# Kernel tuning notes

Measured on AMD Instinct MI355X. Metric: run time of the kernel, lower is better.

## Reference

```python
import jax, jax.numpy as jnp
import numpy as np

N = 100000      # nodes
E = 1600000     # edges (avg degree 16)
EMB = 128
L = 3           # num_layers
NUM_OPS = 64
MAX_BW = 64     # max_bitwidth
P = 4           # max_num_params


def setup_inputs() -> dict:
    key = jax.random.key(0)
    ks = jax.random.split(key, 24)
    w = lambda k, s: jax.random.normal(k, s, jnp.float32) * 0.05
    return {
        "ops": jax.random.randint(ks[0], (N,), 0, NUM_OPS),
        "params": jax.random.randint(ks[1], (N, P), 0, MAX_BW),
        "edge_src": jax.random.randint(ks[2], (E,), 0, N),
        "edge_dst": jax.random.randint(ks[3], (E,), 0, N),
        "op_emb_table": w(ks[4], (NUM_OPS, EMB)),
        "param_emb_table": w(ks[5], (MAX_BW, EMB)),
        "opmlp_w1": w(ks[6], ((1 + P) * EMB, EMB)), "opmlp_b1": w(ks[7], (EMB,)),
        "opmlp_w2": w(ks[8], (EMB, EMB)), "opmlp_b2": w(ks[9], (EMB,)),
        "conv_w": w(ks[10], (L, EMB, EMB)), "conv_b": w(ks[11], (L, EMB)),
        "mlp_w1": w(ks[12], (L * EMB, EMB)), "mlp_b1": w(ks[13], (EMB,)),
        "mlp_w2": w(ks[14], (EMB, EMB)), "mlp_b2": w(ks[15], (EMB,)),
        "mlpinv_w1": w(ks[16], (L * EMB, EMB)), "mlpinv_b1": w(ks[17], (EMB,)),
        "mlpinv_w2": w(ks[18], (EMB, EMB)), "mlpinv_b2": w(ks[19], (EMB,)),
        "comb_w": w(ks[20], (2 * EMB, EMB)), "comb_b": w(ks[21], (EMB,)),
    }


def _lrelu(x):
    return jax.nn.leaky_relu(x)  # slope 0.01, matches nn.LeakyReLU default


def _gin_mean(feat, src, dst, w, b):
    # DGL GINConv(aggregator='mean', eps=0): apply_func(feat + mean_in_neighbors(feat))
    n = feat.shape[0]
    msg = jax.ops.segment_sum(feat[src], dst, num_segments=n)           # [N, EMB]
    deg = jax.ops.segment_sum(jnp.ones(src.shape, feat.dtype), dst, num_segments=n)
    agg = msg / jnp.maximum(deg, 1.0)[:, None]
    return _lrelu((feat + agg) @ w + b)


def reference(ops, params, edge_src, edge_dst,
              op_emb_table, param_emb_table,
              opmlp_w1, opmlp_b1, opmlp_w2, opmlp_b2,
              conv_w, conv_b,
              mlp_w1, mlp_b1, mlp_w2, mlp_b2,
              mlpinv_w1, mlpinv_b1, mlpinv_w2, mlpinv_b2,
              comb_w, comb_b):
    n = ops.shape[0]
    # OpEmb: cat([op_emb] + per-param embs) -> MLP
    op_e = op_emb_table[ops]                               # [N, EMB]
    par_e = param_emb_table[params].reshape(n, -1)         # [N, P*EMB]
    h = jnp.concatenate([op_e, par_e], axis=1)
    h = _lrelu(h @ opmlp_w1 + opmlp_b1) @ opmlp_w2 + opmlp_b2
    states = h
    states_inv = h  # op_emb called twice on same inputs in the original

    conv_outs = []
    for i in range(L):
        states = _gin_mean(states, edge_src, edge_dst, conv_w[i], conv_b[i])
        conv_outs.append(states.sum(axis=0))
    final_sum = states.sum(axis=0)

    conv_outs_inv = []
    for i in range(L):
        states_inv = _gin_mean(states_inv, edge_dst, edge_src, conv_w[i], conv_b[i])
        # NOTE: original code appends states.sum(dim=0) (the final forward states),
        # not states_inv -- faithfully reproduced.
        conv_outs_inv.append(final_sum)

    g_emb = _lrelu(jnp.concatenate(conv_outs) @ mlp_w1 + mlp_b1) @ mlp_w2 + mlp_b2
    g_inv_emb = _lrelu(jnp.concatenate(conv_outs_inv) @ mlpinv_w1 + mlpinv_b1) @ mlpinv_w2 + mlpinv_b2

    out1 = jnp.concatenate([g_emb, g_inv_emb]) @ comb_w + comb_b          # [EMB]
    out2 = jnp.concatenate([states, states_inv], axis=1) @ comb_w + comb_b  # [N, EMB]
    return (out1, out2)
```

## Files before the change

kernel.cpp:

```cpp
#include <hip/hip_runtime.h>


typedef unsigned int  uint;
typedef unsigned short ushort;
typedef float  f32x4  __attribute__((ext_vector_type(4)));
typedef short  bf16x8 __attribute__((ext_vector_type(8)));

#define ABITS 9
#define CAPB  12288
#define CHUNK 2048

__device__ __forceinline__ float lrelu(float x) { return x > 0.0f ? x : 0.01f * x; }
__device__ __forceinline__ ushort f2b(float x) {
    uint u = __float_as_uint(x);
    return (ushort)((u + 0x7fffu + ((u >> 16) & 1u)) >> 16);
}
__device__ __forceinline__ float lof(uint u) { return __uint_as_float(u << 16); }
__device__ __forceinline__ float hif(uint u) { return __uint_as_float(u & 0xffff0000u); }

__global__ void tables_kernel(const float* __restrict__ opT, const float* __restrict__ parT,
                              const float* __restrict__ W1, float* __restrict__ A)
{
    int b = blockIdx.x;
    int t = b >> 6, v = b & 63, j = threadIdx.x;
    const float* emb = (t == 0 ? opT : parT) + v * 128;
    const float* w = W1 + (size_t)t * 128 * 128;
    float acc = 0.f;
    for (int k = 0; k < 128; ++k) acc += emb[k] * w[k * 128 + j];
    A[(size_t)b * 128 + j] = acc;
}

__global__ void prep_w(const float* __restrict__ convw, const float* __restrict__ ow2,
                       const float* __restrict__ cw, ushort* __restrict__ Wt)
{
    int t = blockIdx.x * 256 + threadIdx.x;
    int img = t >> 14, idx = t & 16383;
    int k = idx >> 7, c = idx & 127;
    const float* src;
    if (img < 3)      src = convw + img * 16384;
    else if (img == 3) src = ow2;
    else              src = cw + (img - 4) * 16384;
    float v = src[k * 128 + c];
    int byteoff = (img << 15) + (c << 8) + ((((k >> 3) ^ (c & 7)) << 4)) + ((k & 7) << 1);
    Wt[byteoff >> 1] = f2b(v);
}

__global__ __launch_bounds__(256) void binpass_kernel(
    const int* __restrict__ esrc, const int* __restrict__ edst, int E, int nb,
    int* __restrict__ gcur, uint2* __restrict__ binbuf)
{
    __shared__ int hist[448];
    __shared__ int lstart[448];
    __shared__ int gbase[448];
    __shared__ int lcur[448];
    __shared__ int gsum[8];
    __shared__ uint sKey[CHUNK * 2];
    __shared__ uint sPay[CHUNK * 2];
    __shared__ ushort sBin[CHUNK * 2];
    int tid = threadIdx.x, lane = tid & 63;
    int nb2 = nb * 2;

    for (int chunk = blockIdx.x; (size_t)chunk * CHUNK < (size_t)E; chunk += gridDim.x) {
        int base = chunk * CHUNK;
        int cnt = min(CHUNK, E - base);
        for (int i = tid; i < 448; i += 256) hist[i] = 0;
        __syncthreads();
        int s[8], d[8];
        #pragma unroll
        for (int i = 0; i < 8; ++i) {
            int idx = i * 256 + tid;
            if (idx < cnt) {
                s[i] = esrc[base + idx];
                d[i] = edst[base + idx];
                atomicAdd(&hist[d[i] >> ABITS], 1);
                atomicAdd(&hist[nb + (s[i] >> ABITS)], 1);
            } else s[i] = -1;
        }
        __syncthreads();
        #pragma unroll
        for (int k = 0; k < 2; ++k) {
            int idx = k * 256 + tid;
            int v = (idx < 448) ? hist[idx] : 0;
            int p = v;
            #pragma unroll
            for (int sh = 1; sh < 64; sh <<= 1) { int t = __shfl_up(p, sh, 64); if (lane >= sh) p += t; }
            if (idx < 448) {
                lstart[idx] = p - v;
                if (lane == 63) gsum[idx >> 6] = p;
            }
        }
        __syncthreads();
        if (tid == 0) { int run = 0; for (int g = 0; g < 7; ++g) { int t = gsum[g]; gsum[g] = run; run += t; } }
        __syncthreads();
        #pragma unroll
        for (int k = 0; k < 2; ++k) {
            int idx = k * 256 + tid;
            if (idx < 448) lstart[idx] += gsum[idx >> 6];
        }
        __syncthreads();
        for (int i = tid; i < nb2; i += 256) {
            int h = hist[i];
            gbase[i] = h ? atomicAdd(&gcur[i], h) : 0;
            lcur[i] = lstart[i];
        }
        __syncthreads();
        #pragma unroll
        for (int i = 0; i < 8; ++i) {
            if (s[i] >= 0) {
                int bf = d[i] >> ABITS;
                int p = atomicAdd(&lcur[bf], 1);
                sKey[p] = (uint)d[i]; sPay[p] = (uint)s[i]; sBin[p] = (ushort)bf;
                int bi = nb + (s[i] >> ABITS);
                int q = atomicAdd(&lcur[bi], 1);
                sKey[q] = (uint)s[i]; sPay[q] = (uint)d[i]; sBin[q] = (ushort)bi;
            }
        }
        __syncthreads();
        int total = 2 * cnt;
        for (int p = tid; p < total; p += 256) {
            int b = sBin[p];
            int pos = gbase[b] + (p - lstart[b]);
            if (pos < CAPB) binbuf[(size_t)b * CAPB + pos] = make_uint2(sKey[p], sPay[p]);
        }
        __syncthreads();
    }
}

__global__ __launch_bounds__(256) void csrpass_kernel(
    const uint2* __restrict__ binbuf, const int* __restrict__ gcur, int nb, int N,
    int* __restrict__ csr_f, int* __restrict__ off_f, int* __restrict__ cnt_f,
    int* __restrict__ csr_i, int* __restrict__ off_i, int* __restrict__ cnt_i)
{
    __shared__ int hist[512];
    __shared__ int loff[512];
    __shared__ int cur[512];
    __shared__ int gsum[8];
    int b = blockIdx.x;
    int dir = (b >= nb) ? 1 : 0;
    int binLocal = dir ? b - nb : b;
    int node0 = binLocal << ABITS;
    int nn = min(512, N - node0);
    int tid = threadIdx.x, lane = tid & 63;
    int total = min(gcur[b], CAPB);
    const uint2* seg = binbuf + (size_t)b * CAPB;
    int* csr = dir ? csr_i : csr_f;
    int* off = dir ? off_i : off_f;
    int* cnt = dir ? cnt_i : cnt_f;

    for (int i = tid; i < 512; i += 256) hist[i] = 0;
    __syncthreads();
    for (int e = tid; e < total; e += 256) {
        uint2 kp = seg[e];
        atomicAdd(&hist[kp.x - (uint)node0], 1);
    }
    __syncthreads();
    #pragma unroll
    for (int k = 0; k < 2; ++k) {
        int idx = k * 256 + tid;
        int v = hist[idx];
        int p = v;
        #pragma unroll
        for (int sh = 1; sh < 64; sh <<= 1) { int t = __shfl_up(p, sh, 64); if (lane >= sh) p += t; }
        loff[idx] = p - v;
        if (lane == 63) gsum[idx >> 6] = p;
    }
    __syncthreads();
    if (tid == 0) { int run = 0; for (int g = 0; g < 8; ++g) { int t = gsum[g]; gsum[g] = run; run += t; } }
    __syncthreads();
    #pragma unroll
    for (int k = 0; k < 2; ++k) {
        int idx = k * 256 + tid;
        loff[idx] += gsum[idx >> 6];
    }
    __syncthreads();
    int csrBase = binLocal * CAPB;
    for (int i = tid; i < 512; i += 256) {
        cur[i] = loff[i];
        if (i < nn) { off[node0 + i] = csrBase + loff[i]; cnt[node0 + i] = hist[i]; }
    }
    __syncthreads();
    int* csrSeg = csr + csrBase;
    for (int e = tid; e < total; e += 256) {
        uint2 kp = seg[e];
        int p = atomicAdd(&cur[kp.x - (uint)node0], 1);
        csrSeg[p] = (int)(kp.y << 8);
    }
}

__global__ __launch_bounds__(256, 8) void agg2_kernel(
    const ushort* __restrict__ Sf, const ushort* __restrict__ Si,
    const int* __restrict__ csr_f, const int* __restrict__ off_f, const int* __restrict__ cnt_f,
    const int* __restrict__ csr_i, const int* __restrict__ off_i, const int* __restrict__ cnt_i,
    ushort* __restrict__ msgf, ushort* __restrict__ msgi, int N)
{
    int gw = (blockIdx.x * 256 + threadIdx.x) >> 6;
    int lane = threadIdx.x & 63;
    int dir = 0, g = gw;
    if (g >= N) { dir = 1; g -= N; if (g >= N) return; }
    const char* Sp = (const char*)(dir ? Si : Sf);
    const int* csr = dir ? csr_i : csr_f;
    int off = (dir ? off_i : off_f)[g];
    int deg = (dir ? cnt_i : cnt_f)[g];
    int half = lane >> 5;
    int lb = (lane & 31) << 3;

    float a0 = 0.f, a1 = 0.f, a2 = 0.f, a3 = 0.f;
    int d = 0;
    for (; d + 8 <= deg; d += 8) {
        int b0 = csr[off + d + 0 + half];
        int b1 = csr[off + d + 2 + half];
        int b2 = csr[off + d + 4 + half];
        int b3 = csr[off + d + 6 + half];
        uint2 v0 = *(const uint2*)(Sp + (uint)(b0 + lb));
        uint2 v1 = *(const uint2*)(Sp + (uint)(b1 + lb));
        uint2 v2 = *(const uint2*)(Sp + (uint)(b2 + lb));
        uint2 v3 = *(const uint2*)(Sp + (uint)(b3 + lb));
        a0 += (lof(v0.x) + lof(v1.x)) + (lof(v2.x) + lof(v3.x));
        a1 += (hif(v0.x) + hif(v1.x)) + (hif(v2.x) + hif(v3.x));
        a2 += (lof(v0.y) + lof(v1.y)) + (lof(v2.y) + lof(v3.y));
        a3 += (hif(v0.y) + hif(v1.y)) + (hif(v2.y) + hif(v3.y));
    }
    for (; d + 2 <= deg; d += 2) {
        int b = csr[off + d + half];
        uint2 v = *(const uint2*)(Sp + (uint)(b + lb));
        a0 += lof(v.x); a1 += hif(v.x); a2 += lof(v.y); a3 += hif(v.y);
    }
    if (d < deg && half == 0) {
        int b = csr[off + d];
        uint2 v = *(const uint2*)(Sp + (uint)(b + lb));
        a0 += lof(v.x); a1 += hif(v.x); a2 += lof(v.y); a3 += hif(v.y);
    }
    a0 += __shfl_xor(a0, 32);
    a1 += __shfl_xor(a1, 32);
    a2 += __shfl_xor(a2, 32);
    a3 += __shfl_xor(a3, 32);
    float invd = 1.0f / fmaxf((float)deg, 1.0f);
    uint2 self = *(const uint2*)(Sp + ((size_t)g << 8) + lb);
    a0 = lof(self.x) + a0 * invd;
    a1 = hif(self.x) + a1 * invd;
    a2 = lof(self.y) + a2 * invd;
    a3 = hif(self.y) + a3 * invd;
    if (half == 0) {
        uint2 pk;
        pk.x = (uint)f2b(a0) | ((uint)f2b(a1) << 16);
        pk.y = (uint)f2b(a2) | ((uint)f2b(a3) << 16);
        *(uint2*)((char*)(dir ? msgi : msgf) + ((size_t)g << 8) + lb) = pk;
    }
}

__device__ __forceinline__ void stage_w(const ushort* __restrict__ img, ushort* ldsW, int tid)
{
    const uint4* s = (const uint4*)img;
    uint4* d = (uint4*)ldsW;
    #pragma unroll
    for (int i = 0; i < 4; ++i) d[tid + (i << 9)] = s[tid + (i << 9)];
}

__global__ __launch_bounds__(512, 8) void gemm2_kernel(
    const ushort* __restrict__ msgf, const ushort* __restrict__ msgi,
    ushort* __restrict__ Sf_out, ushort* __restrict__ Si_out,
    const ushort* __restrict__ Wimg, const float* __restrict__ bias,
    float* __restrict__ colsum, int N)
{
    __shared__ __align__(16) ushort ldsW[16384];
    __shared__ float ldsCS[128];
    int tid = threadIdx.x, lane = tid & 63, w = tid >> 6;
    bool fwd = (blockIdx.x & 1) == 0;
    int node0 = (blockIdx.x >> 1) << 7;
    const ushort* msg = fwd ? msgf : msgi;
    ushort* Sout = fwd ? Sf_out : Si_out;

    stage_w(Wimg, ldsW, tid);
    if (fwd && tid < 128) ldsCS[tid] = 0.f;
    __syncthreads();

    int l15 = lane & 15, lg = lane >> 4;
    int node = node0 + (w << 4) + l15;
    int gr = min(node, N - 1);
    const char* Bb = (const char*)msg + ((size_t)gr << 8);

    f32x4 acc[8];
    #pragma unroll
    for (int i = 0; i < 8; ++i) acc[i] = f32x4{0.f, 0.f, 0.f, 0.f};
    #pragma unroll
    for (int kk = 0; kk < 4; ++kk) {
        bf16x8 bfr = *(const bf16x8*)(Bb + (((kk << 2) + lg) << 4));
        #pragma unroll
        for (int ct = 0; ct < 8; ++ct) {
            int c = (ct << 4) + l15;
            const char* Ab = (const char*)ldsW + c * 256;
            bf16x8 af = *(const bf16x8*)(Ab + ((((kk << 2) + lg) << 4) ^ ((c & 7) << 4)));
            acc[ct] = __builtin_amdgcn_mfma_f32_16x16x32_bf16(af, bfr, acc[ct], 0, 0, 0);
        }
    }

    bool valid = node < N;
    #pragma unroll
    for (int ct = 0; ct < 8; ++ct) {
        int ch0 = (ct << 4) + (lg << 2);
        float4 bb = *(const float4*)(bias + ch0);
        float o0 = lrelu(acc[ct][0] + bb.x);
        float o1 = lrelu(acc[ct][1] + bb.y);
        float o2 = lrelu(acc[ct][2] + bb.z);
        float o3 = lrelu(acc[ct][3] + bb.w);
        if (valid) {
            uint2 pk;
            pk.x = (uint)f2b(o0) | ((uint)f2b(o1) << 16);
            pk.y = (uint)f2b(o2) | ((uint)f2b(o3) << 16);
            *(uint2*)((char*)Sout + ((size_t)node << 8) + (ch0 << 1)) = pk;
        }
        if (fwd) {
            float c0 = valid ? o0 : 0.f, c1 = valid ? o1 : 0.f;
            float c2 = valid ? o2 : 0.f, c3 = valid ? o3 : 0.f;
            #pragma unroll
            for (int m = 1; m < 16; m <<= 1) {
                c0 += __shfl_xor(c0, m);
                c1 += __shfl_xor(c1, m);
                c2 += __shfl_xor(c2, m);
                c3 += __shfl_xor(c3, m);
            }
            if (l15 == 0) {
                atomicAdd(&ldsCS[ch0 + 0], c0);
                atomicAdd(&ldsCS[ch0 + 1], c1);
                atomicAdd(&ldsCS[ch0 + 2], c2);
                atomicAdd(&ldsCS[ch0 + 3], c3);
            }
        }
    }
    if (fwd) {
        __syncthreads();
        if (tid < 128) atomicAdd(&colsum[tid], ldsCS[tid]);
    }
}

__global__ __launch_bounds__(512, 4) void opemb_fused(
    const int* __restrict__ ops, const int* __restrict__ params,
    const float* __restrict__ Atab, const float* __restrict__ b1,
    const ushort* __restrict__ W2img, const float* __restrict__ b2,
    ushort* __restrict__ S0, int N)
{
    __shared__ __align__(16) ushort ldsW[16384];
    __shared__ __align__(16) ushort ldsA[16384];
    int tid = threadIdx.x, lane = tid & 63, w = tid >> 6;
    int node0 = blockIdx.x << 7;

    stage_w(W2img, ldsW, tid);

    int r = tid >> 2, sub = tid & 3;
    int g = node0 + r;
    float4 acc4[8];
    if (g < N) {
        int op = ops[g];
        const float4* T = (const float4*)(Atab + ((size_t)op << 7) + (sub << 5));
        #pragma unroll
        for (int q = 0; q < 8; ++q) acc4[q] = T[q];
        #pragma unroll
        for (int p = 0; p < 4; ++p) {
            int pv = params[(g << 2) + p];
            const float4* Tp = (const float4*)(Atab + ((size_t)((p + 1) * 64 + pv) << 7) + (sub << 5));
            #pragma unroll
            for (int q = 0; q < 8; ++q) {
                float4 u = Tp[q];
                acc4[q].x += u.x; acc4[q].y += u.y; acc4[q].z += u.z; acc4[q].w += u.w;
            }
        }
        const float4* Bv = (const float4*)(b1 + (sub << 5));
        #pragma unroll
        for (int q = 0; q < 8; ++q) {
            float4 bb = Bv[q];
            acc4[q].x = lrelu(acc4[q].x + bb.x);
            acc4[q].y = lrelu(acc4[q].y + bb.y);
            acc4[q].z = lrelu(acc4[q].z + bb.z);
            acc4[q].w = lrelu(acc4[q].w + bb.w);
        }
    } else {
        #pragma unroll
        for (int q = 0; q < 8; ++q) acc4[q] = make_float4(0.f, 0.f, 0.f, 0.f);
    }
    int akey = r & 7;
    #pragma unroll
    for (int q2 = 0; q2 < 4; ++q2) {
        int ch = (sub << 2) + q2;
        float4 a = acc4[q2 * 2], b = acc4[q2 * 2 + 1];
        uint4 pk;
        pk.x = (uint)f2b(a.x) | ((uint)f2b(a.y) << 16);
        pk.y = (uint)f2b(a.z) | ((uint)f2b(a.w) << 16);
        pk.z = (uint)f2b(b.x) | ((uint)f2b(b.y) << 16);
        pk.w = (uint)f2b(b.z) | ((uint)f2b(b.w) << 16);
        *(uint4*)((char*)ldsA + r * 256 + ((ch ^ akey) << 4)) = pk;
    }
    __syncthreads();

    int l15 = lane & 15, lg = lane >> 4;
    int node = node0 + (w << 4) + l15;
    int brow = (w << 4) + l15;
    const char* Bb = (const char*)ldsA + brow * 256;
    int bkey = (brow & 7) << 4;
    f32x4 acc[8];
    #pragma unroll
    for (int i = 0; i < 8; ++i) acc[i] = f32x4{0.f, 0.f, 0.f, 0.f};
    #pragma unroll
    for (int kk = 0; kk < 4; ++kk) {
        bf16x8 bfr = *(const bf16x8*)(Bb + ((((kk << 2) + lg) << 4) ^ bkey));
        #pragma unroll
        for (int ct = 0; ct < 8; ++ct) {
            int c = (ct << 4) + l15;
            const char* Ab = (const char*)ldsW + c * 256;
            bf16x8 af = *(const bf16x8*)(Ab + ((((kk << 2) + lg) << 4) ^ ((c & 7) << 4)));
            acc[ct] = __builtin_amdgcn_mfma_f32_16x16x32_bf16(af, bfr, acc[ct], 0, 0, 0);
        }
    }
    if (node < N) {
        #pragma unroll
        for (int ct = 0; ct < 8; ++ct) {
            int ch0 = (ct << 4) + (lg << 2);
            float4 bb = *(const float4*)(b2 + ch0);
            uint2 pk;
            pk.x = (uint)f2b(acc[ct][0] + bb.x) | ((uint)f2b(acc[ct][1] + bb.y) << 16);
            pk.y = (uint)f2b(acc[ct][2] + bb.z) | ((uint)f2b(acc[ct][3] + bb.w) << 16);
            *(uint2*)((char*)S0 + ((size_t)node << 8) + (ch0 << 1)) = pk;
        }
    }
}

__device__ __forceinline__ void final_body(
    float* lds, const float* __restrict__ convsum,
    const float* __restrict__ mw1, const float* __restrict__ mb1,
    const float* __restrict__ mw2, const float* __restrict__ mb2,
    const float* __restrict__ iw1, const float* __restrict__ ib1,
    const float* __restrict__ iw2, const float* __restrict__ ib2,
    const float* __restrict__ cw, const float* __restrict__ cb,
    float* __restrict__ out1)
{
    float* x  = lds;
    float* pa = lds + 384;
    float* pb = lds + 896;
    float* t1 = lds + 1408;
    float* t2 = lds + 1536;
    int tid = threadIdx.x, j = tid & 127, s = tid >> 7;
    if (tid < 384) x[tid] = convsum[tid];
    __syncthreads();
    float a = 0.f, c = 0.f;
    for (int k = s * 96; k < s * 96 + 96; ++k) {
        a += x[k] * mw1[k * 128 + j];
        c += x[256 + (k & 127)] * iw1[k * 128 + j];
    }
    pa[tid] = a; pb[tid] = c;
    __syncthreads();
    if (s == 0) {
        t1[j] = lrelu(pa[j] + pa[128 + j] + pa[256 + j] + pa[384 + j] + mb1[j]);
        t2[j] = lrelu(pb[j] + pb[128 + j] + pb[256 + j] + pb[384 + j] + ib1[j]);
    }
    __syncthreads();
    float b = 0.f, d = 0.f;
    for (int k = s * 32; k < s * 32 + 32; ++k) {
        b += t1[k] * mw2[k * 128 + j];
        d += t2[k] * iw2[k * 128 + j];
    }
    pa[tid] = b; pb[tid] = d;
    __syncthreads();
    if (s == 0) {
        t1[j] = pa[j] + pa[128 + j] + pa[256 + j] + pa[384 + j] + mb2[j];
        t2[j] = pb[j] + pb[128 + j] + pb[256 + j] + pb[384 + j] + ib2[j];
    }
    __syncthreads();
    float e = 0.f;
    for (int k = s * 32; k < s * 32 + 32; ++k)
        e += t1[k] * cw[k * 128 + j] + t2[k] * cw[(128 + k) * 128 + j];
    pa[tid] = e;
    __syncthreads();
    if (s == 0) out1[j] = pa[j] + pa[128 + j] + pa[256 + j] + pa[384 + j] + cb[j];
}

__global__ __launch_bounds__(512, 4) void out2_fused(
    const ushort* __restrict__ Sf, const ushort* __restrict__ Si,
    const ushort* __restrict__ CWimg, const float* __restrict__ cb,
    float* __restrict__ out, int gemmBlocks, int N,
    const float* __restrict__ convsum,
    const float* __restrict__ mw1, const float* __restrict__ mb1,
    const float* __restrict__ mw2, const float* __restrict__ mb2,
    const float* __restrict__ iw1, const float* __restrict__ ib1,
    const float* __restrict__ iw2, const float* __restrict__ ib2,
    const float* __restrict__ cw, float* __restrict__ out1)
{
    __shared__ __align__(16) ushort ldsW[16384];
    int tid = threadIdx.x, lane = tid & 63, w = tid >> 6;
    if ((int)blockIdx.x >= gemmBlocks) {
        final_body((float*)ldsW, convsum, mw1, mb1, mw2, mb2,
                   iw1, ib1, iw2, ib2, cw, cb, out1);
        return;
    }
    int node0 = blockIdx.x << 7;
    int l15 = lane & 15, lg = lane >> 4;
    int node = node0 + (w << 4) + l15;
    int gr = min(node, N - 1);
    f32x4 acc[8];
    #pragma unroll
    for (int i = 0; i < 8; ++i) acc[i] = f32x4{0.f, 0.f, 0.f, 0.f};
    #pragma unroll
    for (int pass = 0; pass < 2; ++pass) {
        if (pass) __syncthreads();
        stage_w(CWimg + (pass << 14), ldsW, tid);
        __syncthreads();
        const char* Bb = (const char*)(pass ? Si : Sf) + ((size_t)gr << 8);
        #pragma unroll
        for (int kk = 0; kk < 4; ++kk) {
            bf16x8 bfr = *(const bf16x8*)(Bb + (((kk << 2) + lg) << 4));
            #pragma unroll
            for (int ct = 0; ct < 8; ++ct) {
                int c = (ct << 4) + l15;
                const char* Ab = (const char*)ldsW + c * 256;
                bf16x8 af = *(const bf16x8*)(Ab + ((((kk << 2) + lg) << 4) ^ ((c & 7) << 4)));
                acc[ct] = __builtin_amdgcn_mfma_f32_16x16x32_bf16(af, bfr, acc[ct], 0, 0, 0);
            }
        }
    }
    if (node < N) {
        #pragma unroll
        for (int ct = 0; ct < 8; ++ct) {
            int ch0 = (ct << 4) + (lg << 2);
            float4 bb = *(const float4*)(cb + ch0);
            float4 o;
            o.x = acc[ct][0] + bb.x;
            o.y = acc[ct][1] + bb.y;
            o.z = acc[ct][2] + bb.z;
            o.w = acc[ct][3] + bb.w;
            *(float4*)(out + (size_t)node * 128 + ch0) = o;
        }
    }
}

extern "C" void kernel_launch(void* const* d_in, const int* in_sizes, int n_in,
                              void* d_out, int out_size, void* d_ws, size_t ws_size,
                              hipStream_t stream)
{
    (void)n_in; (void)out_size; (void)ws_size;
    const int*   ops    = (const int*)d_in[0];
    const int*   params = (const int*)d_in[1];
    const int*   esrc   = (const int*)d_in[2];
    const int*   edst   = (const int*)d_in[3];
    const float* opT    = (const float*)d_in[4];
    const float* parT   = (const float*)d_in[5];
    const float* ow1    = (const float*)d_in[6];
    const float* ob1    = (const float*)d_in[7];
    const float* ow2    = (const float*)d_in[8];
    const float* ob2    = (const float*)d_in[9];
    const float* convw  = (const float*)d_in[10];
    const float* convb  = (const float*)d_in[11];
    const float* mw1    = (const float*)d_in[12];
    const float* mb1    = (const float*)d_in[13];
    const float* mw2    = (const float*)d_in[14];
    const float* mb2    = (const float*)d_in[15];
    const float* iw1    = (const float*)d_in[16];
    const float* ib1    = (const float*)d_in[17];
    const float* iw2    = (const float*)d_in[18];
    const float* ib2    = (const float*)d_in[19];
    const float* cw     = (const float*)d_in[20];
    const float* cb     = (const float*)d_in[21];

    const int N = in_sizes[0];
    const int E = in_sizes[2];
    const int nb = (N + 511) >> ABITS;
    const size_t NP = (size_t)N * 128;

    ushort* S0   = (ushort*)d_ws;
    ushort* S1   = S0 + NP;
    ushort* S2   = S1 + NP;
    ushort* S3   = S2 + NP;
    ushort* Wt   = S3 + NP;
    float*  Atab = (float*)(Wt + 6 * 16384);
    float*  convsum = Atab + 320 * 128;
    int*    gcur = (int*)(convsum + 512);
    uint2*  binbuf = (uint2*)(gcur + 512);
    int*    csr_f = (int*)(binbuf + (size_t)2 * nb * CAPB);
    int*    csr_i = csr_f + (size_t)nb * CAPB;
    int*    off_f = csr_i + (size_t)nb * CAPB;
    int*    cnt_f = off_f + N;
    int*    off_i = cnt_f + N;
    int*    cnt_i = off_i + N;

    float* out1 = (float*)d_out;
    float* out2 = out1 + 128;
    ushort* MSGF = (ushort*)out2;
    ushort* MSGI = MSGF + NP;

    hipMemsetAsync(convsum, 0, sizeof(float) * 1024, stream);

    tables_kernel<<<320, 128, 0, stream>>>(opT, parT, ow1, Atab);
    prep_w<<<384, 256, 0, stream>>>(convw, ow2, cw, Wt);
    binpass_kernel<<<(E + CHUNK - 1) / CHUNK, 256, 0, stream>>>(esrc, edst, E, nb, gcur, binbuf);
    csrpass_kernel<<<2 * nb, 256, 0, stream>>>(binbuf, gcur, nb, N,
                                               csr_f, off_f, cnt_f, csr_i, off_i, cnt_i);

    const int grid = (N + 127) / 128;
    opemb_fused<<<grid, 512, 0, stream>>>(ops, params, Atab, ob1, Wt + 3 * 16384, ob2, S0, N);

    const int aggGrid = (2 * N + 3) / 4;
    agg2_kernel<<<aggGrid, 256, 0, stream>>>(S0, S0, csr_f, off_f, cnt_f, csr_i, off_i, cnt_i, MSGF, MSGI, N);
    gemm2_kernel<<<2 * grid, 512, 0, stream>>>(MSGF, MSGI, S1, S3, Wt,             convb,       convsum,       N);
    agg2_kernel<<<aggGrid, 256, 0, stream>>>(S1, S3, csr_f, off_f, cnt_f, csr_i, off_i, cnt_i, MSGF, MSGI, N);
    gemm2_kernel<<<2 * grid, 512, 0, stream>>>(MSGF, MSGI, S0, S2, Wt + 16384,     convb + 128, convsum + 128, N);
    agg2_kernel<<<aggGrid, 256, 0, stream>>>(S0, S2, csr_f, off_f, cnt_f, csr_i, off_i, cnt_i, MSGF, MSGI, N);
    gemm2_kernel<<<2 * grid, 512, 0, stream>>>(MSGF, MSGI, S1, S3, Wt + 2 * 16384, convb + 256, convsum + 256, N);

    out2_fused<<<grid + 1, 512, 0, stream>>>(S1, S3, Wt + 4 * 16384, cb, out2, grid, N,
                                             convsum, mw1, mb1, mw2, mb2,
                                             iw1, ib1, iw2, ib2, cw, out1);
}
```

Measured before the change: 675.4 us.

## Merge preprocessing kernels into two heterogeneous launches to cut launch overhead

```diff
diff --git a/kernel.cpp b/kernel.cpp
--- a/kernel.cpp
+++ b/kernel.cpp
@@ -18,36 +18,13 @@
 __device__ __forceinline__ float lof(uint u) { return __uint_as_float(u << 16); }
 __device__ __forceinline__ float hif(uint u) { return __uint_as_float(u & 0xffff0000u); }
 
-__global__ void tables_kernel(const float* __restrict__ opT, const float* __restrict__ parT,
-                              const float* __restrict__ W1, float* __restrict__ A)
-{
-    int b = blockIdx.x;
-    int t = b >> 6, v = b & 63, j = threadIdx.x;
-    const float* emb = (t == 0 ? opT : parT) + v * 128;
-    const float* w = W1 + (size_t)t * 128 * 128;
-    float acc = 0.f;
-    for (int k = 0; k < 128; ++k) acc += emb[k] * w[k * 128 + j];
-    A[(size_t)b * 128 + j] = acc;
-}
-
-__global__ void prep_w(const float* __restrict__ convw, const float* __restrict__ ow2,
-                       const float* __restrict__ cw, ushort* __restrict__ Wt)
-{
-    int t = blockIdx.x * 256 + threadIdx.x;
-    int img = t >> 14, idx = t & 16383;
-    int k = idx >> 7, c = idx & 127;
-    const float* src;
-    if (img < 3)      src = convw + img * 16384;
-    else if (img == 3) src = ow2;
-    else              src = cw + (img - 4) * 16384;
-    float v = src[k * 128 + c];
-    int byteoff = (img << 15) + (c << 8) + ((((k >> 3) ^ (c & 7)) << 4)) + ((k & 7) << 1);
-    Wt[byteoff >> 1] = f2b(v);
-}
-
-__global__ __launch_bounds__(256) void binpass_kernel(
-    const int* __restrict__ esrc, const int* __restrict__ edst, int E, int nb,
-    int* __restrict__ gcur, uint2* __restrict__ binbuf)
+__global__ __launch_bounds__(256) void buildprep_kernel(
+    const int* __restrict__ esrc, const int* __restrict__ edst, int E, int nb, int nChunks,
+    int* __restrict__ gcur, uint2* __restrict__ binbuf,
+    const float* __restrict__ opT, const float* __restrict__ parT,
+    const float* __restrict__ W1, float* __restrict__ Atab,
+    const float* __restrict__ convw, const float* __restrict__ ow2,
+    const float* __restrict__ cw, ushort* __restrict__ Wt)
 {
     __shared__ int hist[448];
     __shared__ int lstart[448];
@@ -58,132 +35,239 @@
     __shared__ uint sPay[CHUNK * 2];
     __shared__ ushort sBin[CHUNK * 2];
     int tid = threadIdx.x, lane = tid & 63;
+
+    if ((int)blockIdx.x >= nChunks) {
+        int rb = (int)blockIdx.x - nChunks;
+        if (rb < 160) {
+            int b = (rb << 1) | (tid >> 7);
+            int t = b >> 6, v = b & 63, j = tid & 127;
+            const float* emb = (t == 0 ? opT : parT) + v * 128;
+            const float* w = W1 + (size_t)t * 128 * 128;
+            float acc = 0.f;
+            for (int k = 0; k < 128; ++k) acc += emb[k] * w[k * 128 + j];
+            Atab[(size_t)b * 128 + j] = acc;
+        } else {
+            int t = (rb - 160) * 256 + tid;
+            int img = t >> 14, idx = t & 16383;
+            int k = idx >> 7, c = idx & 127;
+            const float* src;
+            if (img < 3)       src = convw + img * 16384;
+            else if (img == 3) src = ow2;
+            else               src = cw + (img - 4) * 16384;
+            float v = src[k * 128 + c];
+            int byteoff = (img << 15) + (c << 8) + ((((k >> 3) ^ (c & 7)) << 4)) + ((k & 7) << 1);
+            Wt[byteoff >> 1] = f2b(v);
+        }
+        return;
+    }
+
     int nb2 = nb * 2;
-
-    for (int chunk = blockIdx.x; (size_t)chunk * CHUNK < (size_t)E; chunk += gridDim.x) {
-        int base = chunk * CHUNK;
-        int cnt = min(CHUNK, E - base);
-        for (int i = tid; i < 448; i += 256) hist[i] = 0;
-        __syncthreads();
-        int s[8], d[8];
-        #pragma unroll
-        for (int i = 0; i < 8; ++i) {
-            int idx = i * 256 + tid;
-            if (idx < cnt) {
-                s[i] = esrc[base + idx];
-                d[i] = edst[base + idx];
-                atomicAdd(&hist[d[i] >> ABITS], 1);
-                atomicAdd(&hist[nb + (s[i] >> ABITS)], 1);
-            } else s[i] = -1;
-        }
-        __syncthreads();
-        #pragma unroll
-        for (int k = 0; k < 2; ++k) {
-            int idx = k * 256 + tid;
-            int v = (idx < 448) ? hist[idx] : 0;
-            int p = v;
-            #pragma unroll
-            for (int sh = 1; sh < 64; sh <<= 1) { int t = __shfl_up(p, sh, 64); if (lane >= sh) p += t; }
-            if (idx < 448) {
-                lstart[idx] = p - v;
-                if (lane == 63) gsum[idx >> 6] = p;
-            }
-        }
-        __syncthreads();
-        if (tid == 0) { int run = 0; for (int g = 0; g < 7; ++g) { int t = gsum[g]; gsum[g] = run; run += t; } }
-        __syncthreads();
-        #pragma unroll
-        for (int k = 0; k < 2; ++k) {
-            int idx = k * 256 + tid;
-            if (idx < 448) lstart[idx] += gsum[idx >> 6];
-        }
-        __syncthreads();
-        for (int i = tid; i < nb2; i += 256) {
-            int h = hist[i];
-            gbase[i] = h ? atomicAdd(&gcur[i], h) : 0;
-            lcur[i] = lstart[i];
-        }
-        __syncthreads();
-        #pragma unroll
-        for (int i = 0; i < 8; ++i) {
-            if (s[i] >= 0) {
-                int bf = d[i] >> ABITS;
-                int p = atomicAdd(&lcur[bf], 1);
-                sKey[p] = (uint)d[i]; sPay[p] = (uint)s[i]; sBin[p] = (ushort)bf;
-                int bi = nb + (s[i] >> ABITS);
-                int q = atomicAdd(&lcur[bi], 1);
-                sKey[q] = (uint)s[i]; sPay[q] = (uint)d[i]; sBin[q] = (ushort)bi;
-            }
-        }
-        __syncthreads();
-        int total = 2 * cnt;
-        for (int p = tid; p < total; p += 256) {
-            int b = sBin[p];
-            int pos = gbase[b] + (p - lstart[b]);
-            if (pos < CAPB) binbuf[(size_t)b * CAPB + pos] = make_uint2(sKey[p], sPay[p]);
-        }
-        __syncthreads();
-    }
-}
-
-__global__ __launch_bounds__(256) void csrpass_kernel(
+    int base = (int)blockIdx.x * CHUNK;
+    int cnt = min(CHUNK, E - base);
+    for (int i = tid; i < 448; i += 256) hist[i] = 0;
+    __syncthreads();
+    int s[8], d[8];
+    #pragma unroll
+    for (int i = 0; i < 8; ++i) {
+        int idx = i * 256 + tid;
+        if (idx < cnt) {
+            s[i] = esrc[base + idx];
+            d[i] = edst[base + idx];
+            atomicAdd(&hist[d[i] >> ABITS], 1);
+            atomicAdd(&hist[nb + (s[i] >> ABITS)], 1);
+        } else s[i] = -1;
+    }
+    __syncthreads();
+    #pragma unroll
+    for (int k = 0; k < 2; ++k) {
+        int idx = k * 256 + tid;
+        int v = (idx < 448) ? hist[idx] : 0;
+        int p = v;
+        #pragma unroll
+        for (int sh = 1; sh < 64; sh <<= 1) { int t = __shfl_up(p, sh, 64); if (lane >= sh) p += t; }
+        if (idx < 448) {
+            lstart[idx] = p - v;
+            if (lane == 63) gsum[idx >> 6] = p;
+        }
+    }
+    __syncthreads();
+    if (tid == 0) { int run = 0; for (int g = 0; g < 7; ++g) { int t = gsum[g]; gsum[g] = run; run += t; } }
+    __syncthreads();
+    #pragma unroll
+    for (int k = 0; k < 2; ++k) {
+        int idx = k * 256 + tid;
+        if (idx < 448) lstart[idx] += gsum[idx >> 6];
+    }
+    __syncthreads();
+    for (int i = tid; i < nb2; i += 256) {
+        int h = hist[i];
+        gbase[i] = h ? atomicAdd(&gcur[i], h) : 0;
+        lcur[i] = lstart[i];
+    }
+    __syncthreads();
+    #pragma unroll
+    for (int i = 0; i < 8; ++i) {
+        if (s[i] >= 0) {
+            int bf = d[i] >> ABITS;
+            int p = atomicAdd(&lcur[bf], 1);
+            sKey[p] = (uint)d[i]; sPay[p] = (uint)s[i]; sBin[p] = (ushort)bf;
+            int bi = nb + (s[i] >> ABITS);
+            int q = atomicAdd(&lcur[bi], 1);
+            sKey[q] = (uint)s[i]; sPay[q] = (uint)d[i]; sBin[q] = (ushort)bi;
+        }
+    }
+    __syncthreads();
+    int total = 2 * cnt;
+    for (int p = tid; p < total; p += 256) {
+        int b = sBin[p];
+        int pos = gbase[b] + (p - lstart[b]);
+        if (pos < CAPB) binbuf[(size_t)b * CAPB + pos] = make_uint2(sKey[p], sPay[p]);
+    }
+}
+
+__device__ __forceinline__ void stage_w(const ushort* __restrict__ img, ushort* ldsW, int tid)
+{
+    const uint4* s = (const uint4*)img;
+    uint4* d = (uint4*)ldsW;
+    #pragma unroll
+    for (int i = 0; i < 4; ++i) d[tid + (i << 9)] = s[tid + (i << 9)];
+}
+
+__global__ __launch_bounds__(512, 2) void mid_kernel(
     const uint2* __restrict__ binbuf, const int* __restrict__ gcur, int nb, int N,
     int* __restrict__ csr_f, int* __restrict__ off_f, int* __restrict__ cnt_f,
-    int* __restrict__ csr_i, int* __restrict__ off_i, int* __restrict__ cnt_i)
-{
-    __shared__ int hist[512];
-    __shared__ int loff[512];
-    __shared__ int cur[512];
-    __shared__ int gsum[8];
-    int b = blockIdx.x;
-    int dir = (b >= nb) ? 1 : 0;
-    int binLocal = dir ? b - nb : b;
-    int node0 = binLocal << ABITS;
-    int nn = min(512, N - node0);
-    int tid = threadIdx.x, lane = tid & 63;
-    int total = min(gcur[b], CAPB);
-    const uint2* seg = binbuf + (size_t)b * CAPB;
-    int* csr = dir ? csr_i : csr_f;
-    int* off = dir ? off_i : off_f;
-    int* cnt = dir ? cnt_i : cnt_f;
-
-    for (int i = tid; i < 512; i += 256) hist[i] = 0;
-    __syncthreads();
-    for (int e = tid; e < total; e += 256) {
-        uint2 kp = seg[e];
-        atomicAdd(&hist[kp.x - (uint)node0], 1);
-    }
-    __syncthreads();
-    #pragma unroll
-    for (int k = 0; k < 2; ++k) {
-        int idx = k * 256 + tid;
-        int v = hist[idx];
+    int* __restrict__ csr_i, int* __restrict__ off_i, int* __restrict__ cnt_i,
+    const int* __restrict__ ops, const int* __restrict__ params,
+    const float* __restrict__ Atab, const float* __restrict__ b1,
+    const ushort* __restrict__ W2img, const float* __restrict__ b2,
+    ushort* __restrict__ S0)
+{
+    __shared__ __align__(16) ushort ldsW[16384];
+    __shared__ __align__(16) ushort ldsA[16384];
+    int tid = threadIdx.x, lane = tid & 63, w = tid >> 6;
+    int nb2 = 2 * nb;
+
+    if ((int)blockIdx.x < nb2) {
+        int* hist = (int*)ldsA;
+        int* cur  = hist + 512;
+        int* gsum = cur + 512;
+        int b = blockIdx.x;
+        int dir = (b >= nb) ? 1 : 0;
+        int binLocal = dir ? b - nb : b;
+        int node0 = binLocal << ABITS;
+        int nn = min(512, N - node0);
+        int total = min(gcur[b], CAPB);
+        const uint2* seg = binbuf + (size_t)b * CAPB;
+        int* csr = dir ? csr_i : csr_f;
+        int* off = dir ? off_i : off_f;
+        int* cnt = dir ? cnt_i : cnt_f;
+
+        hist[tid] = 0;
+        __syncthreads();
+        for (int e = tid; e < total; e += 512) {
+            uint2 kp = seg[e];
+            atomicAdd(&hist[kp.x - (uint)node0], 1);
+        }
+        __syncthreads();
+        int v = hist[tid];
         int p = v;
         #pragma unroll
         for (int sh = 1; sh < 64; sh <<= 1) { int t = __shfl_up(p, sh, 64); if (lane >= sh) p += t; }
-        loff[idx] = p - v;
-        if (lane == 63) gsum[idx >> 6] = p;
-    }
-    __syncthreads();
-    if (tid == 0) { int run = 0; for (int g = 0; g < 8; ++g) { int t = gsum[g]; gsum[g] = run; run += t; } }
-    __syncthreads();
-    #pragma unroll
-    for (int k = 0; k < 2; ++k) {
-        int idx = k * 256 + tid;
-        loff[idx] += gsum[idx >> 6];
-    }
-    __syncthreads();
-    int csrBase = binLocal * CAPB;
-    for (int i = tid; i < 512; i += 256) {
-        cur[i] = loff[i];
-        if (i < nn) { off[node0 + i] = csrBase + loff[i]; cnt[node0 + i] = hist[i]; }
-    }
-    __syncthreads();
-    int* csrSeg = csr + csrBase;
-    for (int e = tid; e < total; e += 256) {
-        uint2 kp = seg[e];
-        int p = atomicAdd(&cur[kp.x - (uint)node0], 1);
-        csrSeg[p] = (int)(kp.y << 8);
+        if (lane == 63) gsum[w] = p;
+        __syncthreads();
+        if (tid == 0) { int run = 0; for (int g = 0; g < 8; ++g) { int t = gsum[g]; gsum[g] = run; run += t; } }
+        __syncthreads();
+        int lv = p - v + gsum[w];
+        cur[tid] = lv;
+        int csrBase = binLocal * CAPB;
+        if (tid < nn) { off[node0 + tid] = csrBase + lv; cnt[node0 + tid] = v; }
+        __syncthreads();
+        int* csrSeg = csr + csrBase;
+        for (int e = tid; e < total; e += 512) {
+            uint2 kp = seg[e];
+            int q = atomicAdd(&cur[kp.x - (uint)node0], 1);
+            csrSeg[q] = (int)(kp.y << 8);
+        }
+        return;
+    }
+
+    int node0 = ((int)blockIdx.x - nb2) << 7;
+    stage_w(W2img, ldsW, tid);
+
+    int r = tid >> 2, sub = tid & 3;
+    int g = node0 + r;
+    float4 acc4[8];
+    if (g < N) {
+        int op = ops[g];
+        const float4* T = (const float4*)(Atab + ((size_t)op << 7) + (sub << 5));
+        #pragma unroll
+        for (int q = 0; q < 8; ++q) acc4[q] = T[q];
+        #pragma unroll
+        for (int p = 0; p < 4; ++p) {
+            int pv = params[(g << 2) + p];
+            const float4* Tp = (const float4*)(Atab + ((size_t)((p + 1) * 64 + pv) << 7) + (sub << 5));
+            #pragma unroll
+            for (int q = 0; q < 8; ++q) {
+                float4 u = Tp[q];
+                acc4[q].x += u.x; acc4[q].y += u.y; acc4[q].z += u.z; acc4[q].w += u.w;
+            }
+        }
+        const float4* Bv = (const float4*)(b1 + (sub << 5));
+        #pragma unroll
+        for (int q = 0; q < 8; ++q) {
+            float4 bb = Bv[q];
+            acc4[q].x = lrelu(acc4[q].x + bb.x);
+            acc4[q].y = lrelu(acc4[q].y + bb.y);
+            acc4[q].z = lrelu(acc4[q].z + bb.z);
+            acc4[q].w = lrelu(acc4[q].w + bb.w);
+        }
+    } else {
+        #pragma unroll
+        for (int q = 0; q < 8; ++q) acc4[q] = make_float4(0.f, 0.f, 0.f, 0.f);
+    }
+    int akey = r & 7;
+    #pragma unroll
+    for (int q2 = 0; q2 < 4; ++q2) {
+        int ch = (sub << 2) + q2;
+        float4 a = acc4[q2 * 2], b = acc4[q2 * 2 + 1];
+        uint4 pk;
+        pk.x = (uint)f2b(a.x) | ((uint)f2b(a.y) << 16);
+        pk.y = (uint)f2b(a.z) | ((uint)f2b(a.w) << 16);
+        pk.z = (uint)f2b(b.x) | ((uint)f2b(b.y) << 16);
+        pk.w = (uint)f2b(b.z) | ((uint)f2b(b.w) << 16);
+        *(uint4*)((char*)ldsA + r * 256 + ((ch ^ akey) << 4)) = pk;
+    }
+    __syncthreads();
+
+    int l15 = lane & 15, lg = lane >> 4;
+    int node = node0 + (w << 4) + l15;
+    int brow = (w << 4) + l15;
+    const char* Bb = (const char*)ldsA + brow * 256;
+    int bkey = (brow & 7) << 4;
+    f32x4 acc[8];
+    #pragma unroll
+    for (int i = 0; i < 8; ++i) acc[i] = f32x4{0.f, 0.f, 0.f, 0.f};
+    #pragma unroll
+    for (int kk = 0; kk < 4; ++kk) {
+        bf16x8 bfr = *(const bf16x8*)(Bb + ((((kk << 2) + lg) << 4) ^ bkey));
+        #pragma unroll
+        for (int ct = 0; ct < 8; ++ct) {
+            int c = (ct << 4) + l15;
+            const char* Ab = (const char*)ldsW + c * 256;
+            bf16x8 af = *(const bf16x8*)(Ab + ((((kk << 2) + lg) << 4) ^ ((c & 7) << 4)));
+            acc[ct] = __builtin_amdgcn_mfma_f32_16x16x32_bf16(af, bfr, acc[ct], 0, 0, 0);
+        }
+    }
+    if (node < N) {
+        #pragma unroll
+        for (int ct = 0; ct < 8; ++ct) {
+            int ch0 = (ct << 4) + (lg << 2);
+            float4 bb = *(const float4*)(b2 + ch0);
+            uint2 pk;
+            pk.x = (uint)f2b(acc[ct][0] + bb.x) | ((uint)f2b(acc[ct][1] + bb.y) << 16);
+            pk.y = (uint)f2b(acc[ct][2] + bb.z) | ((uint)f2b(acc[ct][3] + bb.w) << 16);
+            *(uint2*)((char*)S0 + ((size_t)node << 8) + (ch0 << 1)) = pk;
+        }
     }
 }
 
@@ -246,14 +330,6 @@
         pk.y = (uint)f2b(a2) | ((uint)f2b(a3) << 16);
         *(uint2*)((char*)(dir ? msgi : msgf) + ((size_t)g << 8) + lb) = pk;
     }
-}
-
-__device__ __forceinline__ void stage_w(const ushort* __restrict__ img, ushort* ldsW, int tid)
-{
-    const uint4* s = (const uint4*)img;
-    uint4* d = (uint4*)ldsW;
-    #pragma unroll
-    for (int i = 0; i < 4; ++i) d[tid + (i << 9)] = s[tid + (i << 9)];
 }
 
 __global__ __launch_bounds__(512, 8) void gemm2_kernel(
@@ -330,96 +406,6 @@
     if (fwd) {
         __syncthreads();
         if (tid < 128) atomicAdd(&colsum[tid], ldsCS[tid]);
-    }
-}
-
-__global__ __launch_bounds__(512, 4) void opemb_fused(
-    const int* __restrict__ ops, const int* __restrict__ params,
-    const float* __restrict__ Atab, const float* __restrict__ b1,
-    const ushort* __restrict__ W2img, const float* __restrict__ b2,
-    ushort* __restrict__ S0, int N)
-{
-    __shared__ __align__(16) ushort ldsW[16384];
-    __shared__ __align__(16) ushort ldsA[16384];
-    int tid = threadIdx.x, lane = tid & 63, w = tid >> 6;
-    int node0 = blockIdx.x << 7;
-
-    stage_w(W2img, ldsW, tid);
-
-    int r = tid >> 2, sub = tid & 3;
-    int g = node0 + r;
-    float4 acc4[8];
-    if (g < N) {
-        int op = ops[g];
-        const float4* T = (const float4*)(Atab + ((size_t)op << 7) + (sub << 5));
-        #pragma unroll
-        for (int q = 0; q < 8; ++q) acc4[q] = T[q];
-        #pragma unroll
-        for (int p = 0; p < 4; ++p) {
-            int pv = params[(g << 2) + p];
-            const float4* Tp = (const float4*)(Atab + ((size_t)((p + 1) * 64 + pv) << 7) + (sub << 5));
-            #pragma unroll
-            for (int q = 0; q < 8; ++q) {
-                float4 u = Tp[q];
-                acc4[q].x += u.x; acc4[q].y += u.y; acc4[q].z += u.z; acc4[q].w += u.w;
-            }
-        }
-        const float4* Bv = (const float4*)(b1 + (sub << 5));
-        #pragma unroll
-        for (int q = 0; q < 8; ++q) {
-            float4 bb = Bv[q];
-            acc4[q].x = lrelu(acc4[q].x + bb.x);
-            acc4[q].y = lrelu(acc4[q].y + bb.y);
-            acc4[q].z = lrelu(acc4[q].z + bb.z);
-            acc4[q].w = lrelu(acc4[q].w + bb.w);
-        }
-    } else {
-        #pragma unroll
-        for (int q = 0; q < 8; ++q) acc4[q] = make_float4(0.f, 0.f, 0.f, 0.f);
-    }
-    int akey = r & 7;
-    #pragma unroll
-    for (int q2 = 0; q2 < 4; ++q2) {
-        int ch = (sub << 2) + q2;
-        float4 a = acc4[q2 * 2], b = acc4[q2 * 2 + 1];
-        uint4 pk;
-        pk.x = (uint)f2b(a.x) | ((uint)f2b(a.y) << 16);
-        pk.y = (uint)f2b(a.z) | ((uint)f2b(a.w) << 16);
-        pk.z = (uint)f2b(b.x) | ((uint)f2b(b.y) << 16);
-        pk.w = (uint)f2b(b.z) | ((uint)f2b(b.w) << 16);
-        *(uint4*)((char*)ldsA + r * 256 + ((ch ^ akey) << 4)) = pk;
-    }
-    __syncthreads();
-
-    int l15 = lane & 15, lg = lane >> 4;
-    int node = node0 + (w << 4) + l15;
-    int brow = (w << 4) + l15;
-    const char* Bb = (const char*)ldsA + brow * 256;
-    int bkey = (brow & 7) << 4;
-    f32x4 acc[8];
-    #pragma unroll
-    for (int i = 0; i < 8; ++i) acc[i] = f32x4{0.f, 0.f, 0.f, 0.f};
-    #pragma unroll
-    for (int kk = 0; kk < 4; ++kk) {
-        bf16x8 bfr = *(const bf16x8*)(Bb + ((((kk << 2) + lg) << 4) ^ bkey));
-        #pragma unroll
-        for (int ct = 0; ct < 8; ++ct) {
-            int c = (ct << 4) + l15;
-            const char* Ab = (const char*)ldsW + c * 256;
-            bf16x8 af = *(const bf16x8*)(Ab + ((((kk << 2) + lg) << 4) ^ ((c & 7) << 4)));
-            acc[ct] = __builtin_amdgcn_mfma_f32_16x16x32_bf16(af, bfr, acc[ct], 0, 0, 0);
-        }
-    }
-    if (node < N) {
-        #pragma unroll
-        for (int ct = 0; ct < 8; ++ct) {
-            int ch0 = (ct << 4) + (lg << 2);
-            float4 bb = *(const float4*)(b2 + ch0);
-            uint2 pk;
-            pk.x = (uint)f2b(acc[ct][0] + bb.x) | ((uint)f2b(acc[ct][1] + bb.y) << 16);
-            pk.y = (uint)f2b(acc[ct][2] + bb.z) | ((uint)f2b(acc[ct][3] + bb.w) << 16);
-            *(uint2*)((char*)S0 + ((size_t)node << 8) + (ch0 << 1)) = pk;
-        }
     }
 }
 
@@ -586,14 +572,16 @@
 
     hipMemsetAsync(convsum, 0, sizeof(float) * 1024, stream);
 
-    tables_kernel<<<320, 128, 0, stream>>>(opT, parT, ow1, Atab);
-    prep_w<<<384, 256, 0, stream>>>(convw, ow2, cw, Wt);
-    binpass_kernel<<<(E + CHUNK - 1) / CHUNK, 256, 0, stream>>>(esrc, edst, E, nb, gcur, binbuf);
-    csrpass_kernel<<<2 * nb, 256, 0, stream>>>(binbuf, gcur, nb, N,
-                                               csr_f, off_f, cnt_f, csr_i, off_i, cnt_i);
+    const int nChunks = (E + CHUNK - 1) / CHUNK;
+    buildprep_kernel<<<nChunks + 160 + 384, 256, 0, stream>>>(
+        esrc, edst, E, nb, nChunks, gcur, binbuf,
+        opT, parT, ow1, Atab, convw, ow2, cw, Wt);
 
     const int grid = (N + 127) / 128;
-    opemb_fused<<<grid, 512, 0, stream>>>(ops, params, Atab, ob1, Wt + 3 * 16384, ob2, S0, N);
+    mid_kernel<<<2 * nb + grid, 512, 0, stream>>>(
+        binbuf, gcur, nb, N,
+        csr_f, off_f, cnt_f, csr_i, off_i, cnt_i,
+        ops, params, Atab, ob1, Wt + 3 * 16384, ob2, S0);
 
     const int aggGrid = (2 * N + 3) / 4;
     agg2_kernel<<<aggGrid, 256, 0, stream>>>(S0, S0, csr_f, off_f, cnt_f, csr_i, off_i, cnt_i, MSGF, MSGI, N);
```

New measurement: 655.3 us. -3.0%, faster.
